# Kernel optimization log

Measured on AMD Instinct MI355X. Metric: run time of the kernel, lower is better.

Reference implementation:

```python
import jax, jax.numpy as jnp
import numpy as np

B, N, DIM = 32, 64, 512          # batch, mem vecs per utterance, model dim
HEADS, DHEAD = 4, 128            # pattern '1, 4, 8, *' forces 4 heads
INNER = HEADS * DHEAD            # 512
FF = 4 * DIM                     # 2048
J = B * N                        # cross-batch kv length (structural: j == i*b)
TOPK = 64
PATTERN = [1, 4, 8, None]        # lookback per head; None == '*' (no mask)


def setup_inputs() -> dict:
    key = jax.random.key(0)
    ks = jax.random.split(key, 12)
    w = lambda k, sh: jax.random.normal(k, sh, dtype=jnp.float32) * 0.02
    inp = {
        'x': jax.random.normal(ks[0], (B, N, DIM), dtype=jnp.float32),
        'context': jax.random.normal(ks[1], (B, J, DIM), dtype=jnp.float32),
        'ff1_w1': w(ks[2], (DIM, FF)), 'ff1_b1': jnp.zeros((FF,), jnp.float32),
        'ff1_w2': w(ks[3], (FF, DIM)), 'ff1_b2': jnp.zeros((DIM,), jnp.float32),
        'ffkv_w1': w(ks[4], (DIM, FF)), 'ffkv_b1': jnp.zeros((FF,), jnp.float32),
        'ffkv_w2': w(ks[5], (FF, DIM)), 'ffkv_b2': jnp.zeros((DIM,), jnp.float32),
        'wq': w(ks[6], (DIM, INNER)), 'bq': jnp.zeros((INNER,), jnp.float32),
        'wkv': w(ks[7], (DIM, 2 * INNER)), 'bkv': jnp.zeros((2 * INNER,), jnp.float32),
        'wo': w(ks[8], (INNER, DIM)), 'bo': jnp.zeros((DIM,), jnp.float32),
        'ln1_g': jnp.ones((DIM,), jnp.float32), 'ln1_b': jnp.zeros((DIM,), jnp.float32),
        'lnkv_g': jnp.ones((DIM,), jnp.float32), 'lnkv_b': jnp.zeros((DIM,), jnp.float32),
        'lna_g': jnp.ones((DIM,), jnp.float32), 'lna_b': jnp.zeros((DIM,), jnp.float32),
        'lnf_g': jnp.ones((DIM,), jnp.float32), 'lnf_b': jnp.zeros((DIM,), jnp.float32),
    }
    return inp


def _ln(z, g, b):
    m = z.mean(-1, keepdims=True)
    v = ((z - m) ** 2).mean(-1, keepdims=True)
    return g * (z - m) * jax.lax.rsqrt(v + 1e-5) + b


def _swish(z):
    return z * jax.nn.sigmoid(z)


def reference(x, context, ff1_w1, ff1_b1, ff1_w2, ff1_b2,
              ffkv_w1, ffkv_b1, ffkv_w2, ffkv_b2,
              wq, bq, wkv, bkv, wo, bo,
              ln1_g, ln1_b, lnkv_g, lnkv_b, lna_g, lna_b, lnf_g, lnf_b):
    # half-step pre-norm feedforwards (conformer convention) on queries and KV memory
    x = x + 0.5 * (_swish(_ln(x, ln1_g, ln1_b) @ ff1_w1 + ff1_b1) @ ff1_w2 + ff1_b2)
    context = context + 0.5 * (_swish(_ln(context, lnkv_g, lnkv_b) @ ffkv_w1 + ffkv_b1) @ ffkv_w2 + ffkv_b2)

    # cross attention: x [B,N,DIM] attends over cross-batch memory context [B,J,DIM]
    a = _ln(x, lna_g, lna_b)
    q = (a @ wq + bq).reshape(B, N, HEADS, DHEAD).transpose(0, 2, 1, 3)      # bhnd
    k, v = jnp.split(context @ wkv + bkv, 2, axis=-1)
    k = k.reshape(B, J, HEADS, DHEAD).transpose(0, 2, 1, 3)                  # bhjd
    v = v.reshape(B, J, HEADS, DHEAD).transpose(0, 2, 1, 3)
    dots = jnp.einsum('bhid,bhjd->bhij', q, k) * (DHEAD ** -0.5)            # [B,H,N,J]

    NEG = -jnp.finfo(dots.dtype).max
    # sparse top-k masking (keep only values >= k-th largest per row)
    thr = jax.lax.top_k(dots, TOPK)[0][..., -1:]
    dots = jnp.where(dots < thr, NEG, dots)

    # per-head local attention mask over batch index of kv memory vectors
    diff = jnp.abs((jnp.arange(J) // N)[None, :] - jnp.arange(B)[:, None])   # [B,J]
    head_masks = [jnp.ones((B, J), bool) if L is None else (diff <= L) for L in PATTERN]
    local = jnp.stack(head_masks, axis=1)[:, :, None, :]                     # [B,H,1,J]
    dots = jnp.where(local, dots, NEG)

    attn = jax.nn.softmax(dots, axis=-1)
    out = jnp.einsum('bhij,bhjd->bhid', attn, v).transpose(0, 2, 1, 3).reshape(B, N, INNER)
    x = x + out @ wo + bo
    return _ln(x, lnf_g, lnf_b)
```

## Files before the change

### kernel.cpp

```cpp
#include <hip/hip_runtime.h>
#include <math.h>

#define BB     32
#define NN     64
#define DIMM   512
#define HEADS  4
#define DH     128
#define FFD    2048
#define JJ     2048
#define RX     2048
#define TOPKK  64
#define CH     8192
#define NCH    8
#define FLTMAXF 3.402823466e38f

#define WS_WORDS_REQ 82837504ull

typedef unsigned short u16;
typedef unsigned int   u32;

using f32x4  = __attribute__((ext_vector_type(4))) float;
using short8 = __attribute__((ext_vector_type(8))) short;

__device__ __forceinline__ float wred_sum(float v) {
    #pragma unroll
    for (int m = 1; m < 64; m <<= 1) v += __shfl_xor(v, m, 64);
    return v;
}
__device__ __forceinline__ int wred_sumi(int v) {
    #pragma unroll
    for (int m = 1; m < 64; m <<= 1) v += __shfl_xor(v, m, 64);
    return v;
}
__device__ __forceinline__ float wred_max(float v) {
    #pragma unroll
    for (int m = 1; m < 64; m <<= 1) v = fmaxf(v, __shfl_xor(v, m, 64));
    return v;
}
__device__ __forceinline__ unsigned fkey(float f) {
    unsigned u = __float_as_uint(f);
    return (u & 0x80000000u) ? ~u : (u | 0x80000000u);
}

__device__ __forceinline__ u16 bf16rne(float f) {
    u32 u = __float_as_uint(f);
    return (u16)((u + 0x7FFFu + ((u >> 16) & 1u)) >> 16);
}
__device__ __forceinline__ float bf16tof(u16 h) {
    return __uint_as_float(((u32)h) << 16);
}
__device__ __forceinline__ void split2(float f, u16& h, u16& l) {
    h = bf16rne(f);
    l = bf16rne(f - bf16tof(h));
}

__device__ __forceinline__ void gload16(const void* g, void* l) {
    __builtin_amdgcn_global_load_lds(
        (const __attribute__((address_space(1))) void*)g,
        (__attribute__((address_space(3))) void*)l,
        16, 0, 0);
}

__global__ __launch_bounds__(256) void ln_k(const float* __restrict__ in,
                                            const float* __restrict__ gam,
                                            const float* __restrict__ bet,
                                            float* __restrict__ out)
{
    const int row  = blockIdx.x * 4 + (threadIdx.x >> 6);
    const int lane = threadIdx.x & 63;
    const float* p = in + (size_t)row * DIMM + lane * 8;

    float a[8];
    *(float4*)&a[0] = *(const float4*)p;
    *(float4*)&a[4] = *(const float4*)(p + 4);

    float s = 0.f;
    #pragma unroll
    for (int i = 0; i < 8; ++i) s += a[i];
    s = wred_sum(s);
    const float mean = s * (1.0f / DIMM);

    float vs = 0.f;
    #pragma unroll
    for (int i = 0; i < 8; ++i) { float d = a[i] - mean; vs += d * d; }
    vs = wred_sum(vs);
    const float var = vs * (1.0f / DIMM) + 1e-5f;
    float r = rsqrtf(var);
    r = r * (1.5f - 0.5f * var * r * r);

    float g[8], b[8];
    *(float4*)&g[0] = *(const float4*)(gam + lane * 8);
    *(float4*)&g[4] = *(const float4*)(gam + lane * 8 + 4);
    *(float4*)&b[0] = *(const float4*)(bet + lane * 8);
    *(float4*)&b[4] = *(const float4*)(bet + lane * 8 + 4);

    float o[8];
    #pragma unroll
    for (int i = 0; i < 8; ++i) o[i] = g[i] * (a[i] - mean) * r + b[i];

    float* q = out + (size_t)row * DIMM + lane * 8;
    *(float4*)q       = *(float4*)&o[0];
    *(float4*)(q + 4) = *(float4*)&o[4];
}

__global__ __launch_bounds__(256) void ln_split_k(const float* __restrict__ in,
                                                  const float* __restrict__ gam,
                                                  const float* __restrict__ bet,
                                                  u16* __restrict__ oh,
                                                  u16* __restrict__ ol)
{
    const int row  = blockIdx.x * 4 + (threadIdx.x >> 6);
    const int lane = threadIdx.x & 63;
    const float* p = in + (size_t)row * DIMM + lane * 8;

    float a[8];
    *(float4*)&a[0] = *(const float4*)p;
    *(float4*)&a[4] = *(const float4*)(p + 4);

    float s = 0.f;
    #pragma unroll
    for (int i = 0; i < 8; ++i) s += a[i];
    s = wred_sum(s);
    const float mean = s * (1.0f / DIMM);

    float vs = 0.f;
    #pragma unroll
    for (int i = 0; i < 8; ++i) { float d = a[i] - mean; vs += d * d; }
    vs = wred_sum(vs);
    const float var = vs * (1.0f / DIMM) + 1e-5f;
    float r = rsqrtf(var);
    r = r * (1.5f - 0.5f * var * r * r);

    float g[8], b[8];
    *(float4*)&g[0] = *(const float4*)(gam + lane * 8);
    *(float4*)&g[4] = *(const float4*)(gam + lane * 8 + 4);
    *(float4*)&b[0] = *(const float4*)(bet + lane * 8);
    *(float4*)&b[4] = *(const float4*)(bet + lane * 8 + 4);

    u32 ph[4], pl[4];
    #pragma unroll
    for (int i = 0; i < 4; ++i) {
        float o0 = g[2*i]   * (a[2*i]   - mean) * r + b[2*i];
        float o1 = g[2*i+1] * (a[2*i+1] - mean) * r + b[2*i+1];
        u16 h0, l0, h1, l1;
        split2(o0, h0, l0);
        split2(o1, h1, l1);
        ph[i] = (u32)h0 | ((u32)h1 << 16);
        pl[i] = (u32)l0 | ((u32)l1 << 16);
    }
    uint4 vh; vh.x = ph[0]; vh.y = ph[1]; vh.z = ph[2]; vh.w = ph[3];
    uint4 vl; vl.x = pl[0]; vl.y = pl[1]; vl.z = pl[2]; vl.w = pl[3];
    *(uint4*)(oh + (size_t)row * DIMM + lane * 8) = vh;
    *(uint4*)(ol + (size_t)row * DIMM + lane * 8) = vl;
}

__global__ __launch_bounds__(256) void wsplit_k(const float* __restrict__ W,
                                                u16* __restrict__ Th, u16* __restrict__ Tl,
                                                int K, int N)
{
    __shared__ float t[64][65];
    const int k0 = blockIdx.y * 64, n0 = blockIdx.x * 64;
    const int tid = threadIdx.x;
    #pragma unroll
    for (int p = 0; p < 16; ++p) {
        const int idx = p * 256 + tid;
        const int r = idx >> 6, c = idx & 63;
        t[r][c] = W[(size_t)(k0 + r) * N + n0 + c];
    }
    __syncthreads();
    #pragma unroll
    for (int p = 0; p < 16; ++p) {
        const int idx = p * 256 + tid;
        const int r = idx >> 6, c = idx & 63;
        float v = t[c][r];
        u16 h, l; split2(v, h, l);
        Th[(size_t)(n0 + r) * K + k0 + c] = h;
        Tl[(size_t)(n0 + r) * K + k0 + c] = l;
    }
}

#define SM_SWISH          0
#define SM_RESHALF_F32    1
#define SM_RESHALF_SPLIT  2
#define SM_Q              3
#define SM_KV             4
#define SM_RESBIAS        5

template<int MODE>
__global__ __launch_bounds__(256, 2) void mgemm_k(
    const u16* __restrict__ Ahi, const u16* __restrict__ Alo,
    const u16* __restrict__ Bhi, const u16* __restrict__ Blo,
    const float* __restrict__ bias, const float* __restrict__ res,
    float* __restrict__ o1, u16* __restrict__ o2, u16* __restrict__ o3,
    u16* __restrict__ o4, int N, int K, int row0)
{
    __shared__ u16 sAh[128 * 32], sAl[128 * 32], sBh[128 * 32], sBl[128 * 32];

    const int tid  = threadIdx.x;
    const int nwg  = gridDim.x * gridDim.y;
    int bid = blockIdx.y * gridDim.x + blockIdx.x;
    bid = (bid & 7) * (nwg >> 3) + (bid >> 3);
    const int bm   = (bid / gridDim.x) * 128;
    const int bn   = (bid % gridDim.x) * 128;

    const int lane = tid & 63;
    const int wid  = tid >> 6;
    const int wr   = (wid >> 1) * 64;
    const int wc   = (wid & 1) * 64;
    const int colL = lane & 15;
    const int rowL = (lane >> 4) * 4;
    const int kL   = (lane >> 4) * 8;
    const int srow = lane >> 2;
    const int skc  = (lane & 3) * 8;

    const f32x4 z4 = {0.f, 0.f, 0.f, 0.f};
    f32x4 acc[4][4];
    #pragma unroll
    for (int i = 0; i < 4; ++i)
        #pragma unroll
        for (int j = 0; j < 4; ++j) acc[i][j] = z4;

    for (int k0 = 0; k0 < K; k0 += 32) {
        __syncthreads();
        #pragma unroll
        for (int ss = 0; ss < 2; ++ss) {
            const int s = wid * 2 + ss;
            const int r = s * 16 + srow;
            const size_t ga = (size_t)(bm + r) * K + k0 + skc;
            const size_t gb = (size_t)(bn + r) * K + k0 + skc;
            gload16(&Ahi[ga], &sAh[s * 512]);
            gload16(&Alo[ga], &sAl[s * 512]);
            gload16(&Bhi[gb], &sBh[s * 512]);
            gload16(&Blo[gb], &sBl[s * 512]);
        }
        __syncthreads();

        short8 ah[4], al[4], bh[4], bl[4];
        #pragma unroll
        for (int f = 0; f < 4; ++f) {
            const int ra = (wr + f * 16 + colL) * 32 + kL;
            ah[f] = *(const short8*)&sAh[ra];
            al[f] = *(const short8*)&sAl[ra];
            const int rb = (wc + f * 16 + colL) * 32 + kL;
            bh[f] = *(const short8*)&sBh[rb];
            bl[f] = *(const short8*)&sBl[rb];
        }
        #pragma unroll
        for (int fm = 0; fm < 4; ++fm)
            #pragma unroll
            for (int fn = 0; fn < 4; ++fn) {
                acc[fm][fn] = __builtin_amdgcn_mfma_f32_16x16x32_bf16(ah[fm], bh[fn], acc[fm][fn], 0, 0, 0);
                acc[fm][fn] = __builtin_amdgcn_mfma_f32_16x16x32_bf16(ah[fm], bl[fn], acc[fm][fn], 0, 0, 0);
                acc[fm][fn] = __builtin_amdgcn_mfma_f32_16x16x32_bf16(al[fm], bh[fn], acc[fm][fn], 0, 0, 0);
            }
    }

    float biasc[4];
    #pragma unroll
    for (int fn = 0; fn < 4; ++fn) biasc[fn] = bias[bn + wc + fn * 16 + colL];

    #pragma unroll
    for (int fm = 0; fm < 4; ++fm) {
        #pragma unroll
        for (int fn = 0; fn < 4; ++fn) {
            const int gc = bn + wc + fn * 16 + colL;
            #pragma unroll
            for (int r = 0; r < 4; ++r) {
                const int gr = bm + wr + fm * 16 + rowL + r;
                float o = acc[fm][fn][r] + biasc[fn];
                if (MODE == SM_SWISH) {
                    float s = o / (1.f + expf(-o));
                    u16 h, l; split2(s, h, l);
                    o2[(size_t)gr * N + gc] = h;
                    o3[(size_t)gr * N + gc] = l;
                } else if (MODE == SM_RESHALF_F32) {
                    o1[(size_t)gr * N + gc] = res[(size_t)gr * N + gc] + 0.5f * o;
                } else if (MODE == SM_RESHALF_SPLIT) {
                    float v = res[(size_t)gr * N + gc] + 0.5f * o;
                    u16 h, l; split2(v, h, l);
                    o2[(size_t)gr * N + gc] = h;
                    o3[(size_t)gr * N + gc] = l;
                } else if (MODE == SM_Q) {
                    const int b_ = gr >> 6, i_ = gr & 63, h_ = gc >> 7, d_ = gc & 127;
                    const size_t idx = (((size_t)(b_ * HEADS + h_) * NN + i_) << 7) + d_;
                    u16 h, l; split2(o, h, l);
                    o2[idx] = h; o3[idx] = l;
                } else if (MODE == SM_KV) {
                    const int grow = row0 + gr;
                    const int b_ = grow >> 11, j_ = grow & 2047;
                    if (gc < DIMM) {
                        const int h_ = gc >> 7, d_ = gc & 127;
                        const size_t idx = (((size_t)(b_ * HEADS + h_) * JJ + j_) << 7) + d_;
                        u16 h, l; split2(o, h, l);
                        o2[idx] = h; o3[idx] = l;
                    } else {
                        const int cc2 = gc - DIMM;
                        const int h_ = cc2 >> 7, d_ = cc2 & 127;
                        o4[((size_t)(b_ * HEADS + h_) * DH + d_) * JJ + j_] = bf16rne(o);
                    }
                } else {
                    o1[(size_t)gr * N + gc] = res[(size_t)gr * N + gc] + o;
                }
            }
        }
    }
}

__global__ __launch_bounds__(256, 2) void dmfma_k(
    const u16* __restrict__ Qh, const u16* __restrict__ Ql,
    const u16* __restrict__ Kh, const u16* __restrict__ Kl,
    float* __restrict__ dots)
{
    __shared__ u16 sQh[64 * 32], sQl[64 * 32], sKh[128 * 32], sKl[128 * 32];

    const int tid  = threadIdx.x;
    const int bh   = blockIdx.y;
    const int jt   = blockIdx.x * 128;
    const int lane = tid & 63;
    const int wid  = tid >> 6;
    const int wr   = (wid >> 1) * 32;
    const int wc   = (wid & 1) * 64;
    const int colL = lane & 15;
    const int rowL = (lane >> 4) * 4;
    const int kL   = (lane >> 4) * 8;
    const int srow = lane >> 2;
    const int skc  = (lane & 3) * 8;

    const size_t qbase = (size_t)bh * NN * DH;
    const size_t kbase = (size_t)bh * JJ * DH;

    const f32x4 z4 = {0.f, 0.f, 0.f, 0.f};
    f32x4 acc[2][4];
    #pragma unroll
    for (int i = 0; i < 2; ++i)
        #pragma unroll
        for (int j = 0; j < 4; ++j) acc[i][j] = z4;

    for (int d0 = 0; d0 < DH; d0 += 32) {
        __syncthreads();
        {
            const size_t gq = qbase + (size_t)(wid * 16 + srow) * DH + d0 + skc;
            gload16(&Qh[gq], &sQh[wid * 512]);
            gload16(&Ql[gq], &sQl[wid * 512]);
        }
        #pragma unroll
        for (int ss = 0; ss < 2; ++ss) {
            const int s = wid * 2 + ss;
            const size_t gk = kbase + (size_t)(jt + s * 16 + srow) * DH + d0 + skc;
            gload16(&Kh[gk], &sKh[s * 512]);
            gload16(&Kl[gk], &sKl[s * 512]);
        }
        __syncthreads();

        short8 qh[2], ql[2], kh[4], kl[4];
        #pragma unroll
        for (int f = 0; f < 2; ++f) {
            const int ra = (wr + f * 16 + colL) * 32 + kL;
            qh[f] = *(const short8*)&sQh[ra];
            ql[f] = *(const short8*)&sQl[ra];
        }
        #pragma unroll
        for (int f = 0; f < 4; ++f) {
            const int rb = (wc + f * 16 + colL) * 32 + kL;
            kh[f] = *(const short8*)&sKh[rb];
            kl[f] = *(const short8*)&sKl[rb];
        }
        #pragma unroll
        for (int fm = 0; fm < 2; ++fm)
            #pragma unroll
            for (int fn = 0; fn < 4; ++fn) {
                acc[fm][fn] = __builtin_amdgcn_mfma_f32_16x16x32_bf16(qh[fm], kh[fn], acc[fm][fn], 0, 0, 0);
                acc[fm][fn] = __builtin_amdgcn_mfma_f32_16x16x32_bf16(qh[fm], kl[fn], acc[fm][fn], 0, 0, 0);
                acc[fm][fn] = __builtin_amdgcn_mfma_f32_16x16x32_bf16(ql[fm], kh[fn], acc[fm][fn], 0, 0, 0);
            }
    }

    const float scl = 0.08838834764831845f;
    #pragma unroll
    for (int fm = 0; fm < 2; ++fm)
        #pragma unroll
        for (int fn = 0; fn < 4; ++fn)
            #pragma unroll
            for (int r = 0; r < 4; ++r) {
                const int qi = wr + fm * 16 + rowL + r;
                const int jc = jt + wc + fn * 16 + colL;
                dots[((size_t)bh * NN + qi) * JJ + jc] = acc[fm][fn][r] * scl;
            }
}

__global__ __launch_bounds__(256) void topk_sm_k(float* __restrict__ dots)
{
    const int wid  = threadIdx.x >> 6;
    const int lane = threadIdx.x & 63;
    const int r = blockIdx.x * 4 + wid;
    const int b = r >> 8;
    const int h = (r >> 6) & 3;
    float* row = dots + (size_t)r * JJ;

    float d[32];
    unsigned key[32];
    #pragma unroll
    for (int t = 0; t < 32; ++t) {
        d[t] = row[lane + 64 * t];
        key[t] = fkey(d[t]);
    }

    unsigned cur = 0u;
    for (int bit = 31; bit >= 0; --bit) {
        const unsigned cand = cur | (1u << bit);
        int c = 0;
        #pragma unroll
        for (int t = 0; t < 32; ++t) c += (key[t] >= cand) ? 1 : 0;
        c = wred_sumi(c);
        if (c >= TOPKK) cur = cand;
    }

    const int LB = (h == 0) ? 1 : (h == 1) ? 4 : (h == 2) ? 8 : 1000;
    float m = -FLTMAXF;
    #pragma unroll
    for (int t = 0; t < 32; ++t) {
        const int j = lane + 64 * t;
        int df = (j >> 6) - b; df = (df < 0) ? -df : df;
        const bool keep = (df <= LB) && (key[t] >= cur);
        d[t] = keep ? d[t] : -FLTMAXF;
        m = fmaxf(m, d[t]);
    }
    m = wred_max(m);

    float s = 0.f;
    float e[32];
    #pragma unroll
    for (int t = 0; t < 32; ++t) {
        e[t] = expf(d[t] - m);
        s += e[t];
    }
    s = wred_sum(s);
    const float inv = 1.0f / s;

    u16* prow = (u16*)row;
    #pragma unroll
    for (int t = 0; t < 32; ++t) prow[lane + 64 * t] = bf16rne(e[t] * inv);
}

__global__ __launch_bounds__(256, 2) void pvm_k(
    const u16* __restrict__ Pb,
    const u16* __restrict__ Vt,
    u16* __restrict__ attnh, u16* __restrict__ attnl)
{
    __shared__ u16 sP[64 * 32], sVt[128 * 32];

    const int tid  = threadIdx.x;
    const int bh   = blockIdx.x;
    const int lane = tid & 63;
    const int wid  = tid >> 6;
    const int wr   = (wid >> 1) * 32;
    const int wc   = (wid & 1) * 64;
    const int colL = lane & 15;
    const int rowL = (lane >> 4) * 4;
    const int kL   = (lane >> 4) * 8;
    const int srow = lane >> 2;
    const int skc  = (lane & 3) * 8;

    const size_t pbase = (size_t)bh * NN * (2 * JJ);
    const size_t vbase = (size_t)bh * DH * JJ;

    const f32x4 z4 = {0.f, 0.f, 0.f, 0.f};
    f32x4 acc[2][4];
    #pragma unroll
    for (int i = 0; i < 2; ++i)
        #pragma unroll
        for (int j = 0; j < 4; ++j) acc[i][j] = z4;

    for (int j0 = 0; j0 < JJ; j0 += 32) {
        __syncthreads();
        {
            const size_t gp = pbase + (size_t)(wid * 16 + srow) * (2 * JJ) + j0 + skc;
            gload16(&Pb[gp], &sP[wid * 512]);
        }
        #pragma unroll
        for (int ss = 0; ss < 2; ++ss) {
            const int s = wid * 2 + ss;
            const size_t gv = vbase + (size_t)(s * 16 + srow) * JJ + j0 + skc;
            gload16(&Vt[gv], &sVt[s * 512]);
        }
        __syncthreads();

        short8 pf[2], vf[4];
        #pragma unroll
        for (int f = 0; f < 2; ++f)
            pf[f] = *(const short8*)&sP[(wr + f * 16 + colL) * 32 + kL];
        #pragma unroll
        for (int f = 0; f < 4; ++f)
            vf[f] = *(const short8*)&sVt[(wc + f * 16 + colL) * 32 + kL];
        #pragma unroll
        for (int fm = 0; fm < 2; ++fm)
            #pragma unroll
            for (int fn = 0; fn < 4; ++fn)
                acc[fm][fn] = __builtin_amdgcn_mfma_f32_16x16x32_bf16(pf[fm], vf[fn], acc[fm][fn], 0, 0, 0);
    }

    const int b = bh >> 2, h = bh & 3;
    #pragma unroll
    for (int fm = 0; fm < 2; ++fm)
        #pragma unroll
        for (int fn = 0; fn < 4; ++fn)
            #pragma unroll
            for (int r = 0; r < 4; ++r) {
                const int i = wr + fm * 16 + rowL + r;
                const int dcol = wc + fn * 16 + colL;
                const size_t idx = (size_t)(b * NN + i) * DIMM + h * DH + dcol;
                u16 hh, ll; split2(acc[fm][fn][r], hh, ll);
                attnh[idx] = hh; attnl[idx] = ll;
            }
}

extern "C" void kernel_launch(void* const* d_in, const int* in_sizes, int n_in,
                              void* d_out, int out_size, void* d_ws, size_t ws_size,
                              hipStream_t stream)
{
    if (ws_size < WS_WORDS_REQ * 4ull) return;

    const float* x       = (const float*)d_in[0];
    const float* ctx     = (const float*)d_in[1];
    const float* ff1_w1  = (const float*)d_in[2];
    const float* ff1_b1  = (const float*)d_in[3];
    const float* ff1_w2  = (const float*)d_in[4];
    const float* ff1_b2  = (const float*)d_in[5];
    const float* ffkv_w1 = (const float*)d_in[6];
    const float* ffkv_b1 = (const float*)d_in[7];
    const float* ffkv_w2 = (const float*)d_in[8];
    const float* ffkv_b2 = (const float*)d_in[9];
    const float* wq      = (const float*)d_in[10];
    const float* bq      = (const float*)d_in[11];
    const float* wkv     = (const float*)d_in[12];
    const float* bkv     = (const float*)d_in[13];
    const float* wo      = (const float*)d_in[14];
    const float* bo      = (const float*)d_in[15];
    const float* ln1_g   = (const float*)d_in[16];
    const float* ln1_b   = (const float*)d_in[17];
    const float* lnkv_g  = (const float*)d_in[18];
    const float* lnkv_b  = (const float*)d_in[19];
    const float* lna_g   = (const float*)d_in[20];
    const float* lna_b   = (const float*)d_in[21];
    const float* lnf_g   = (const float*)d_in[22];
    const float* lnf_b   = (const float*)d_in[23];

    float* ws = (float*)d_ws;
    u16*   Qhs = (u16*)ws;
    u16*   Qls = Qhs + 1048576;
    u16*   Khs = (u16*)(ws + 1048576);
    u16*   Kls = Khs + 33554432;
    u16*   Vt  = (u16*)(ws + 34603008);
    float* x1  = ws + 51380224;
    float* wsp = x1 + 1048576;
    float* R   = wsp + 5242880;

    u16* w1Th  = (u16*)wsp;
    u16* w1Tl  = w1Th  + 1048576;
    u16* w2Th  = w1Tl  + 1048576;
    u16* w2Tl  = w2Th  + 1048576;
    u16* kw1Th = w2Tl  + 1048576;
    u16* kw1Tl = kw1Th + 1048576;
    u16* kw2Th = kw1Tl + 1048576;
    u16* kw2Tl = kw2Th + 1048576;
    u16* wqTh  = kw2Tl + 1048576;
    u16* wqTl  = wqTh  + 262144;
    u16* wkvTh = wqTl  + 262144;
    u16* wkvTl = wkvTh + 524288;
    u16* woTh  = wkvTl + 524288;
    u16* woTl  = woTh  + 262144;

    u16* lnxh  = (u16*)R;
    u16* lnxl  = lnxh  + 1048576;
    u16* hxh   = lnxl  + 1048576;
    u16* hxl   = hxh   + 4194304;
    u16* lnx2h = hxl   + 4194304;
    u16* lnx2l = lnx2h + 1048576;
    u16* lnch  = (u16*)R;
    u16* lncl  = lnch  + 4194304;
    u16* hch   = lncl  + 4194304;
    u16* hcl   = hch   + 16777216;
    u16* ctxnh = hcl   + 16777216;
    u16* ctxnl = ctxnh + 4194304;
    float* dots = R;
    float* x2   = R;
    u16* attnh  = (u16*)ws;
    u16* attnl  = attnh + 1048576;

    wsplit_k<<<dim3(FFD / 64, DIMM / 64), 256, 0, stream>>>(ff1_w1,  w1Th,  w1Tl,  DIMM, FFD);
    wsplit_k<<<dim3(DIMM / 64, FFD / 64), 256, 0, stream>>>(ff1_w2,  w2Th,  w2Tl,  FFD,  DIMM);
    wsplit_k<<<dim3(FFD / 64, DIMM / 64), 256, 0, stream>>>(ffkv_w1, kw1Th, kw1Tl, DIMM, FFD);
    wsplit_k<<<dim3(DIMM / 64, FFD / 64), 256, 0, stream>>>(ffkv_w2, kw2Th, kw2Tl, FFD,  DIMM);
    wsplit_k<<<dim3(DIMM / 64, DIMM / 64), 256, 0, stream>>>(wq,     wqTh,  wqTl,  DIMM, DIMM);
    wsplit_k<<<dim3(1024 / 64, DIMM / 64), 256, 0, stream>>>(wkv,    wkvTh, wkvTl, DIMM, 1024);
    wsplit_k<<<dim3(DIMM / 64, DIMM / 64), 256, 0, stream>>>(wo,     woTh,  woTl,  DIMM, DIMM);

    ln_split_k<<<RX / 4, 256, 0, stream>>>(x, ln1_g, ln1_b, lnxh, lnxl);
    mgemm_k<SM_SWISH><<<dim3(FFD / 128, RX / 128), 256, 0, stream>>>(
        lnxh, lnxl, w1Th, w1Tl, ff1_b1, nullptr, nullptr, hxh, hxl, nullptr, FFD, DIMM, 0);
    mgemm_k<SM_RESHALF_F32><<<dim3(DIMM / 128, RX / 128), 256, 0, stream>>>(
        hxh, hxl, w2Th, w2Tl, ff1_b2, x, x1, nullptr, nullptr, nullptr, DIMM, FFD, 0);
    ln_split_k<<<RX / 4, 256, 0, stream>>>(x1, lna_g, lna_b, lnx2h, lnx2l);
    mgemm_k<SM_Q><<<dim3(DIMM / 128, RX / 128), 256, 0, stream>>>(
        lnx2h, lnx2l, wqTh, wqTl, bq, nullptr, nullptr, Qhs, Qls, nullptr, DIMM, DIMM, 0);

    for (int c = 0; c < NCH; ++c) {
        const float* cptr = ctx + (size_t)c * CH * DIMM;
        ln_split_k<<<CH / 4, 256, 0, stream>>>(cptr, lnkv_g, lnkv_b, lnch, lncl);
        mgemm_k<SM_SWISH><<<dim3(FFD / 128, CH / 128), 256, 0, stream>>>(
            lnch, lncl, kw1Th, kw1Tl, ffkv_b1, nullptr, nullptr, hch, hcl, nullptr, FFD, DIMM, 0);
        mgemm_k<SM_RESHALF_SPLIT><<<dim3(DIMM / 128, CH / 128), 256, 0, stream>>>(
            hch, hcl, kw2Th, kw2Tl, ffkv_b2, cptr, nullptr, ctxnh, ctxnl, nullptr, DIMM, FFD, 0);
        mgemm_k<SM_KV><<<dim3(1024 / 128, CH / 128), 256, 0, stream>>>(
            ctxnh, ctxnl, wkvTh, wkvTl, bkv, nullptr, nullptr, Khs, Kls, Vt, 1024, DIMM, c * CH);
    }

    dmfma_k<<<dim3(JJ / 128, BB * HEADS), 256, 0, stream>>>(Qhs, Qls, Khs, Kls, dots);
    topk_sm_k<<<(BB * HEADS * NN) / 4, 256, 0, stream>>>(dots);
    pvm_k<<<BB * HEADS, 256, 0, stream>>>((const u16*)dots, Vt, attnh, attnl);

    mgemm_k<SM_RESBIAS><<<dim3(DIMM / 128, RX / 128), 256, 0, stream>>>(
        attnh, attnl, woTh, woTl, bo, x1, x2, nullptr, nullptr, nullptr, DIMM, DIMM, 0);
    ln_k<<<RX / 4, 256, 0, stream>>>(x2, lnf_g, lnf_b, (float*)d_out);
}
```

Measured before the change: 2.089 ms.

## Double-buffer LDS tiles in the split-bf16 MFMA GEMM main loop

The GEMM kernel now keeps two shared-memory buffers for each of the A/B hi/lo tiles. The next K-tile's global-to-LDS loads are issued before the MFMA work on the current tile, and a scheduling barrier keeps the compiler from reordering them. This replaces two block-wide barriers per iteration with one, so global memory latency can overlap compute. In exchange, LDS use per block doubles to about 64KB, which may limit occupancy against the requested two blocks per CU.

```diff
diff --git a/kernel.cpp b/kernel.cpp
--- a/kernel.cpp
+++ b/kernel.cpp
@@ -194,7 +194,7 @@
     float* __restrict__ o1, u16* __restrict__ o2, u16* __restrict__ o3,
     u16* __restrict__ o4, int N, int K, int row0)
 {
-    __shared__ u16 sAh[128 * 32], sAl[128 * 32], sBh[128 * 32], sBl[128 * 32];
+    __shared__ u16 sAh[2][128 * 32], sAl[2][128 * 32], sBh[2][128 * 32], sBl[2][128 * 32];
 
     const int tid  = threadIdx.x;
     const int nwg  = gridDim.x * gridDim.y;
@@ -220,30 +220,39 @@
         #pragma unroll
         for (int j = 0; j < 4; ++j) acc[i][j] = z4;
 
-    for (int k0 = 0; k0 < K; k0 += 32) {
-        __syncthreads();
-        #pragma unroll
-        for (int ss = 0; ss < 2; ++ss) {
-            const int s = wid * 2 + ss;
-            const int r = s * 16 + srow;
-            const size_t ga = (size_t)(bm + r) * K + k0 + skc;
-            const size_t gb = (size_t)(bn + r) * K + k0 + skc;
-            gload16(&Ahi[ga], &sAh[s * 512]);
-            gload16(&Alo[ga], &sAl[s * 512]);
-            gload16(&Bhi[gb], &sBh[s * 512]);
-            gload16(&Blo[gb], &sBl[s * 512]);
-        }
-        __syncthreads();
+    #define STAGE_TILE(bf, k0)                                                    \
+        {                                                                         \
+            _Pragma("unroll")                                                     \
+            for (int ss = 0; ss < 2; ++ss) {                                      \
+                const int s = wid * 2 + ss;                                       \
+                const int r = s * 16 + srow;                                      \
+                const size_t ga = (size_t)(bm + r) * K + (k0) + skc;              \
+                const size_t gb = (size_t)(bn + r) * K + (k0) + skc;              \
+                gload16(&Ahi[ga], &sAh[bf][s * 512]);                             \
+                gload16(&Alo[ga], &sAl[bf][s * 512]);                             \
+                gload16(&Bhi[gb], &sBh[bf][s * 512]);                             \
+                gload16(&Blo[gb], &sBl[bf][s * 512]);                             \
+            }                                                                     \
+        }
+
+    const int nt = K >> 5;
+    STAGE_TILE(0, 0);
+    __syncthreads();
+
+    int cur = 0;
+    for (int t = 0; t < nt; ++t) {
+        if (t + 1 < nt) STAGE_TILE(cur ^ 1, (t + 1) << 5);
+        __builtin_amdgcn_sched_barrier(0);
 
         short8 ah[4], al[4], bh[4], bl[4];
         #pragma unroll
         for (int f = 0; f < 4; ++f) {
             const int ra = (wr + f * 16 + colL) * 32 + kL;
-            ah[f] = *(const short8*)&sAh[ra];
-            al[f] = *(const short8*)&sAl[ra];
+            ah[f] = *(const short8*)&sAh[cur][ra];
+            al[f] = *(const short8*)&sAl[cur][ra];
             const int rb = (wc + f * 16 + colL) * 32 + kL;
-            bh[f] = *(const short8*)&sBh[rb];
-            bl[f] = *(const short8*)&sBl[rb];
+            bh[f] = *(const short8*)&sBh[cur][rb];
+            bl[f] = *(const short8*)&sBl[cur][rb];
         }
         #pragma unroll
         for (int fm = 0; fm < 4; ++fm)
@@ -253,7 +262,11 @@
                 acc[fm][fn] = __builtin_amdgcn_mfma_f32_16x16x32_bf16(ah[fm], bl[fn], acc[fm][fn], 0, 0, 0);
                 acc[fm][fn] = __builtin_amdgcn_mfma_f32_16x16x32_bf16(al[fm], bh[fn], acc[fm][fn], 0, 0, 0);
             }
-    }
+
+        cur ^= 1;
+        if (t + 1 < nt) __syncthreads();
+    }
+    #undef STAGE_TILE
 
     float biasc[4];
     #pragma unroll
```

Result: no change. 2.116 ms (+1.3%).
